# Kernel optimization log

Hardware: AMD Instinct MI355X
Metric: run time of the kernel (lower is better)

## Reference

```python
import jax, jax.numpy as jnp
import numpy as np

B, R, D = 16, 2048, 512
H2, NREL = 2 * D, 2048  # relation_mlp hidden = 2*d_model, output = n_relations
MIN_PROB = 0.1          # early-stop probability threshold from the torch code


def setup_inputs() -> dict:
    key = jax.random.key(0)
    ks = jax.random.split(key, 8)
    sc = lambda k, shp: jax.random.normal(k, shp, jnp.float32) * 0.02
    return {
        "rel_encoding": jax.random.normal(ks[0], (B, R, D), jnp.float32),
        "na_emb": jax.random.normal(ks[1], (D,), jnp.float32),
        "v_w": sc(ks[2], (D, D)), "v_b": jnp.zeros((D,), jnp.float32),
        "o_w": sc(ks[3], (D, D)), "o_b": jnp.zeros((D,), jnp.float32),
        "ln_g": jnp.ones((D,), jnp.float32), "ln_b": jnp.zeros((D,), jnp.float32),
        "w1": sc(ks[4], (H2, D)), "b1": jnp.zeros((H2,), jnp.float32),
        "w2": sc(ks[5], (NREL, H2)), "b2": jnp.zeros((NREL,), jnp.float32),
    }


def _ln(x, g, b, eps=1e-5):
    m = jnp.mean(x, axis=-1, keepdims=True)
    v = jnp.var(x, axis=-1, keepdims=True)
    return (x - m) * jax.lax.rsqrt(v + eps) * g + b


def reference(rel_encoding, na_emb, v_w, v_b, o_w, o_b, ln_g, ln_b, w1, b1, w2, b2):
    # Cross-attention with a single key/value token: softmax over a length-1 axis
    # is identically 1, so attn_out = out_proj(v_proj(kv)) for every query position.
    x = rel_encoding                                         # [B,R,D]
    attn = (x @ v_w.T + v_b) @ o_w.T + o_b                   # [B,R,D]

    def step_logits(state):                                  # state broadcasts to [B,R,D]
        h = _ln(attn + state, ln_g, ln_b)                    # residual + layernorm
        return jax.nn.relu(h @ w1.T + b1) @ w2.T + b2        # [B,R,NREL]

    # step 0: query is the na_embedding
    p0 = jax.nn.softmax(step_logits(na_emb), axis=-1)
    m0 = jnp.max(p0, axis=-1)
    i0 = jnp.argmax(p0, axis=-1)
    cont0 = (i0 != 0) & (m0 >= MIN_PROB)                     # else break before step 0 emits

    # step 1: last appended state is the relation encoding itself
    p1 = jax.nn.softmax(step_logits(x), axis=-1)
    m1 = jnp.max(p1, axis=-1)
    i1 = jnp.argmax(p1, axis=-1)
    cont1 = cont0 & (i1 != 0) & (m1 >= MIN_PROB)

    # rule_score = prod of accepted step probs; 0.0 if no step accepted
    scores = jnp.where(cont0, jnp.where(cont1, m0 * m1, m0), 0.0)  # [B,R]
    lengths = cont0.astype(jnp.int32) + cont1.astype(jnp.int32)    # ragged rule lengths
    return scores, i0, i1, lengths
```

## Files before the change

kernel.cpp:

```cpp
#include <hip/hip_runtime.h>
#include <math.h>

#define MTOT 32768
#define DD   512
#define HHD  1024
#define NRELN 2048
#define SCA  64.f
#define SCB  1024.f
#define INVS (1.f / 65536.f)
#define CAPR 4096
#define MARGIN 2.0e-3f

typedef _Float16 h8  __attribute__((ext_vector_type(8)));
typedef float    f4  __attribute__((ext_vector_type(4)));
typedef float    f16v __attribute__((ext_vector_type(16)));

__device__ __forceinline__ void fsplit(float x, _Float16& h, _Float16& l) {
  _Float16 t = (_Float16)x;
  h = t;
  l = (_Float16)(x - (float)t);
}

__device__ __forceinline__ void gld16(const _Float16* g, _Float16* l) {
  __builtin_amdgcn_global_load_lds(
      (const __attribute__((address_space(1))) void*)g,
      (__attribute__((address_space(3))) void*)l, 16, 0, 0);
}


__global__ void prep_wvo_split(const float* __restrict__ vw, const float* __restrict__ ow,
                               _Float16* __restrict__ wh, _Float16* __restrict__ wl) {
  int idx = blockIdx.x * 256 + threadIdx.x;
  int k = idx & 511;
  int n = idx >> 9;
  float s = 0.f;
  for (int j = 0; j < DD; ++j) s += ow[n * DD + j] * vw[j * DD + k];
  fsplit(s * SCB, wh[n * DD + k], wl[n * DD + k]);
}

__global__ void prep_cvec(const float* __restrict__ ow, const float* __restrict__ vb,
                          const float* __restrict__ ob, float* __restrict__ c) {
  int i = blockIdx.x * 256 + threadIdx.x;
  if (i < DD) {
    float s = ob[i];
    for (int k = 0; k < DD; ++k) s += ow[i * DD + k] * vb[k];
    c[i] = s;
  }
}

__global__ void prep_w1p_split(const float* __restrict__ w1, const float* __restrict__ g,
                               _Float16* __restrict__ wh, _Float16* __restrict__ wl) {
  int idx = blockIdx.x * 256 + threadIdx.x;
  int k = idx & 511;
  int n = idx >> 9;
  fsplit(w1[n * DD + k] * g[k] * SCB, wh[n * DD + k], wl[n * DD + k]);
}

__global__ void prep_b1p(const float* __restrict__ w1, const float* __restrict__ lnb,
                         const float* __restrict__ b1, float* __restrict__ b1p) {
  int n = blockIdx.x * 256 + threadIdx.x;
  if (n < HHD) {
    float s = b1[n];
    for (int k = 0; k < DD; ++k) s += w1[n * DD + k] * lnb[k];
    b1p[n] = s;
  }
}

__global__ void prep_w2_split(const float* __restrict__ w2,
                              _Float16* __restrict__ wh, _Float16* __restrict__ wl) {
  int idx = blockIdx.x * 256 + threadIdx.x;
  int k = idx & 1023;
  int n = idx >> 10;
  fsplit(w2[n * HHD + k] * SCB, wh[n * HHD + k], wl[n * HHD + k]);
}

__global__ void split_x(const float* __restrict__ src, _Float16* __restrict__ h,
                        _Float16* __restrict__ l) {
  int idx = (blockIdx.x * 256 + threadIdx.x) * 8;
  float4 a = *(const float4*)(src + idx);
  float4 b = *(const float4*)(src + idx + 4);
  float vv[8] = {a.x, a.y, a.z, a.w, b.x, b.y, b.z, b.w};
  _Float16 hh[8], ll[8];
#pragma unroll
  for (int i = 0; i < 8; ++i) fsplit(vv[i] * SCA, hh[i], ll[i]);
  *(h8*)(h + idx) = *(h8*)hh;
  *(h8*)(l + idx) = *(h8*)ll;
}

__global__ void zero_cnt(int* c) { c[blockIdx.x * 256 + threadIdx.x] = 0; }

template <int MODE, int KDIM, int NTOT>
__global__ __launch_bounds__(256) void gemm_split(
    const _Float16* __restrict__ Ah, const _Float16* __restrict__ Al,
    const _Float16* __restrict__ Bh, const _Float16* __restrict__ Bl,
    const float* __restrict__ bias,
    float* __restrict__ outF,
    _Float16* __restrict__ outHh, _Float16* __restrict__ outHl,
    float* __restrict__ pM, float* __restrict__ pI,
    const int* __restrict__ cntp, int pstr) {
  __shared__ __align__(16) _Float16 sA[2][128][32];
  __shared__ __align__(16) _Float16 sB[2][128][32];
  const int t = threadIdx.x;
  const int lane = t & 63;
  const int wv = t >> 6;
  const int wr = wv & 1, wc = wv >> 1;
  const int l31 = lane & 31, half = lane >> 5;
  const int n0 = blockIdx.y << 7;

  const _Float16* gsp = (wv == 0) ? Ah : (wv == 1) ? Al : (wv == 2) ? Bh : Bl;
  _Float16* lbase = (wv == 0) ? &sA[0][0][0] : (wv == 1) ? &sA[1][0][0]
                  : (wv == 2) ? &sB[0][0][0] : &sB[1][0][0];
  const int srow = lane >> 2;
  const int scp = lane & 3;
  const int swzE = ((srow >> 1) & 3) ^ ((srow >> 3) & 1);
  const int swzO = swzE ^ 2;
  const int swz = ((l31 >> 1) ^ (l31 >> 3)) & 3;

  int nmb;
  if constexpr (MODE == 2) {
    int a = *cntp;
    if (a > CAPR) a = CAPR;
    nmb = (a + 127) >> 7;
  } else {
    nmb = gridDim.x;
  }

  for (int mb = blockIdx.x; mb < nmb; mb += gridDim.x) {
    const int m0 = mb << 7;
    const int gb = (wv < 2) ? m0 : n0;
    const _Float16* gA0 = gsp + (size_t)(gb + srow) * KDIM + ((scp ^ swzE) << 3);
    const _Float16* gA1 = gsp + (size_t)(gb + srow) * KDIM + ((scp ^ swzO) << 3);

    f16v acc[2][2] = {};
    for (int k0 = 0; k0 < KDIM; k0 += 32) {
      __syncthreads();
#pragma unroll
      for (int it = 0; it < 8; ++it)
        gld16(((it & 1) ? gA1 : gA0) + (size_t)(it * 16) * KDIM + k0, lbase + it * 512);
      __syncthreads();
#pragma unroll
      for (int ks = 0; ks < 2; ++ks) {
        const int pos = (((ks << 1) + half) ^ swz) << 3;
        h8 af_h[2], af_l[2], bf_h[2], bf_l[2];
#pragma unroll
        for (int i = 0; i < 2; ++i) {
          const int mr = wr * 64 + i * 32 + l31;
          af_h[i] = *(const h8*)&sA[0][mr][pos];
          af_l[i] = *(const h8*)&sA[1][mr][pos];
        }
#pragma unroll
        for (int j = 0; j < 2; ++j) {
          const int nr = wc * 64 + j * 32 + l31;
          bf_h[j] = *(const h8*)&sB[0][nr][pos];
          bf_l[j] = *(const h8*)&sB[1][nr][pos];
        }
#pragma unroll
        for (int j = 0; j < 2; ++j)
#pragma unroll
          for (int i = 0; i < 2; ++i) {
            acc[i][j] = __builtin_amdgcn_mfma_f32_32x32x16_f16(af_h[i], bf_h[j], acc[i][j], 0, 0, 0);
            acc[i][j] = __builtin_amdgcn_mfma_f32_32x32x16_f16(af_h[i], bf_l[j], acc[i][j], 0, 0, 0);
            acc[i][j] = __builtin_amdgcn_mfma_f32_32x32x16_f16(af_l[i], bf_h[j], acc[i][j], 0, 0, 0);
          }
      }
    }

    float bb[2];
    int gc[2];
#pragma unroll
    for (int j = 0; j < 2; ++j) {
      gc[j] = n0 + wc * 64 + j * 32 + l31;
      bb[j] = bias[gc[j]];
    }
    if constexpr (MODE == 0) {
#pragma unroll
      for (int i = 0; i < 2; ++i)
#pragma unroll
        for (int r = 0; r < 16; ++r) {
          const int row = m0 + wr * 64 + i * 32 + (r & 3) + 8 * (r >> 2) + 4 * half;
#pragma unroll
          for (int j = 0; j < 2; ++j)
            outF[(size_t)row * NTOT + gc[j]] = acc[i][j][r] * INVS + bb[j];
        }
    } else if constexpr (MODE == 1) {
#pragma unroll
      for (int i = 0; i < 2; ++i)
#pragma unroll
        for (int r = 0; r < 16; ++r) {
          const int row = m0 + wr * 64 + i * 32 + (r & 3) + 8 * (r >> 2) + 4 * half;
#pragma unroll
          for (int j = 0; j < 2; ++j) {
            float v = fmaxf(acc[i][j][r] * INVS + bb[j], 0.f) * SCA;
            _Float16 hh, ll;
            fsplit(v, hh, ll);
            outHh[(size_t)row * NTOT + gc[j]] = hh;
            outHl[(size_t)row * NTOT + gc[j]] = ll;
          }
        }
    } else {
      const int slot = blockIdx.y * 2 + wc;
#pragma unroll
      for (int i = 0; i < 2; ++i)
#pragma unroll
        for (int r = 0; r < 16; ++r) {
          float v0 = acc[i][0][r] * INVS + bb[0];
          float v1 = acc[i][1][r] * INVS + bb[1];
          float M;
          int I;
          if (v0 >= v1) { M = v0; I = gc[0]; }
          else          { M = v1; I = gc[1]; }
#pragma unroll
          for (int sh = 1; sh <= 16; sh <<= 1) {
            float M2 = __shfl_xor(M, sh);
            int   I2 = __shfl_xor(I, sh);
            if (M2 > M || (M2 == M && I2 < I)) { M = M2; I = I2; }
          }
          if (l31 == 0) {
            const int grow = m0 + wr * 64 + i * 32 + (r & 3) + 8 * (r >> 2) + 4 * half;
            pM[(size_t)slot * pstr + grow] = M;
            pI[(size_t)slot * pstr + grow] = (float)I;
          }
        }
    }
  }
}


#define SBAR __builtin_amdgcn_s_barrier()
#define SCHB __builtin_amdgcn_sched_barrier(0)
#define LW0  asm volatile("s_waitcnt lgkmcnt(0)" ::: "memory")
#define VW(N) asm volatile("s_waitcnt vmcnt(" #N ")" ::: "memory")
#define VWNONE ((void)0)

#define GLB(k, ktn, nb_)                                                      \
  gld16(Bh + (size_t)(sBb + (k) * 16384 + (ktn) * 64),                        \
        lds + 32768 + dBb + (k) * 1024 + (nb_) * 16384)
#define GLA(k, ktn, nb_)                                                      \
  gld16(Ah + (size_t)(sAb + (k) * 32768 + (ktn) * 64),                        \
        lds + dAb + (k) * 2048 + (nb_) * 16384)

#define PHASE(p, cbuf, STAGE, VWS)                                            \
  {                                                                           \
    h8 a00 = *(const h8*)(lds + (cbuf) + aRow + (2 * (p)) * 1024 + kc0);      \
    h8 a01 = *(const h8*)(lds + (cbuf) + aRow + (2 * (p)) * 1024 + kc1);      \
    h8 a10 = *(const h8*)(lds + (cbuf) + aRow + (2 * (p) + 1) * 1024 + kc0);  \
    h8 a11 = *(const h8*)(lds + (cbuf) + aRow + (2 * (p) + 1) * 1024 + kc1);  \
    STAGE;                                                                    \
    SBAR;                                                                     \
    LW0;                                                                      \
    SCHB;                                                                     \
    __builtin_amdgcn_s_setprio(1);                                            \
    _Pragma("unroll") for (int j = 0; j < 4; ++j) {                           \
      acc[2 * (p)][j] = __builtin_amdgcn_mfma_f32_16x16x32_f16(               \
          a00, bf0[j], acc[2 * (p)][j], 0, 0, 0);                             \
      acc[2 * (p)][j] = __builtin_amdgcn_mfma_f32_16x16x32_f16(               \
          a01, bf1[j], acc[2 * (p)][j], 0, 0, 0);                             \
      acc[2 * (p) + 1][j] = __builtin_amdgcn_mfma_f32_16x16x32_f16(           \
          a10, bf0[j], acc[2 * (p) + 1][j], 0, 0, 0);                         \
      acc[2 * (p) + 1][j] = __builtin_amdgcn_mfma_f32_16x16x32_f16(           \
          a11, bf1[j], acc[2 * (p) + 1][j], 0, 0, 0);                         \
    }                                                                         \
    __builtin_amdgcn_s_setprio(0);                                            \
    VWS;                                                                      \
    SBAR;                                                                     \
  }

__global__ __launch_bounds__(512, 2) void gemm_approx(
    const _Float16* __restrict__ Ah, const _Float16* __restrict__ Bh,
    const float* __restrict__ bias,
    float* __restrict__ pM, float* __restrict__ pM2,
    float* __restrict__ pS, int* __restrict__ pI, int astr) {
  __shared__ __align__(16) _Float16 lds[65536];
  const int t = threadIdx.x;
  const int lane = t & 63;
  const int wv = t >> 6;
  const int wr = wv >> 2;
  const int wc = wv & 3;
  const int q = lane >> 4;
  const int l16 = lane & 15;
  const int s7 = l16 & 7;
  const int l8 = lane >> 3;
  const int lc = lane & 7;

  const int Yg = gridDim.y;
  const int id = blockIdx.x + (blockIdx.y << 3);
  const int g8 = (id >> 6) << 3;
  const int r = id & 63;
  int mb, nb;
  if (g8 + 8 <= Yg) { mb = g8 + (r & 7); nb = r >> 3; }
  else { int rem = Yg - g8; mb = g8 + (r % rem); nb = r / rem; }

  const int m0 = mb << 8;
  const int n0 = nb << 8;

  const int swz8 = (lc ^ l8) << 3;
  const int sBb = (n0 + wc * 64 + wr * 8 + l8) * HHD + swz8;
  const int dBb = (wc * 64 + wr * 8) * 64;
  const int sAb = (m0 + wr * 128 + wc * 8 + l8) * HHD + swz8;
  const int dAb = (wr * 128 + wc * 8) * 64;

  const int kc0 = ((q) ^ s7) << 3;
  const int kc1 = ((q + 4) ^ s7) << 3;
  const int aRow = (wr * 128 + l16) * 64;
  const int bRow = 32768 + (wc * 64 + l16) * 64;

  f4 acc[8][4] = {};

  GLB(0, 0, 0); GLB(1, 0, 0); GLB(2, 0, 0); GLB(3, 0, 0);
  GLA(0, 0, 0); GLA(1, 0, 0); GLA(2, 0, 0); GLA(3, 0, 0);
  VW(3);
  SBAR;

  for (int kt = 0; kt < 15; ++kt) {
    const int cb = (kt & 1) << 14;
    const int nbuf = (kt & 1) ^ 1;
    const int ktn = kt + 1;
    h8 bf0[4], bf1[4];
#pragma unroll
    for (int j = 0; j < 4; ++j) {
      bf0[j] = *(const h8*)(lds + cb + bRow + j * 1024 + kc0);
      bf1[j] = *(const h8*)(lds + cb + bRow + j * 1024 + kc1);
    }
    PHASE(0, cb, GLB(0, ktn, nbuf); GLB(1, ktn, nbuf), VW(4));
    PHASE(1, cb, GLB(2, ktn, nbuf); GLB(3, ktn, nbuf), VW(5));
    PHASE(2, cb, GLA(0, ktn, nbuf); GLA(1, ktn, nbuf), VW(6));
    PHASE(3, cb, GLA(2, ktn, nbuf); GLA(3, ktn, nbuf), VW(3));
  }
  {
    const int cb = 16384;
    h8 bf0[4], bf1[4];
#pragma unroll
    for (int j = 0; j < 4; ++j) {
      bf0[j] = *(const h8*)(lds + cb + bRow + j * 1024 + kc0);
      bf1[j] = *(const h8*)(lds + cb + bRow + j * 1024 + kc1);
    }
    PHASE(0, cb, VWNONE, VW(2));
    PHASE(1, cb, VWNONE, VW(1));
    PHASE(2, cb, VWNONE, VW(0));
    PHASE(3, cb, VWNONE, VWNONE);
  }

  const int slot = nb * 4 + wc;
  float bb[4];
  int gcx[4];
#pragma unroll
  for (int j = 0; j < 4; ++j) {
    gcx[j] = n0 + wc * 64 + j * 16 + l16;
    bb[j] = bias[gcx[j]];
  }
#pragma unroll
  for (int i = 0; i < 8; ++i)
#pragma unroll
    for (int rr = 0; rr < 4; ++rr) {
      float M = acc[i][0][rr] * INVS + bb[0], M2 = -INFINITY, S = 1.f;
      int I = gcx[0];
#pragma unroll
      for (int j = 1; j < 4; ++j) {
        float v = acc[i][j][rr] * INVS + bb[j];
        if (v > M || (v == M && gcx[j] < I)) {
          S = S * __expf(M - v) + 1.f; M2 = M; M = v; I = gcx[j];
        } else {
          S += __expf(v - M); M2 = fmaxf(M2, v);
        }
      }
#pragma unroll
      for (int sh = 1; sh <= 8; sh <<= 1) {
        float Mo = __shfl_xor(M, sh);
        float M2o = __shfl_xor(M2, sh);
        float So = __shfl_xor(S, sh);
        int   Io = __shfl_xor(I, sh);
        if (Mo > M || (Mo == M && Io < I)) {
          S = S * __expf(M - Mo) + So; M2 = fmaxf(M, M2o); M = Mo; I = Io;
        } else {
          S += So * __expf(Mo - M); M2 = fmaxf(M2, Mo);
        }
      }
      if (l16 == 0) {
        const int grow = m0 + wr * 128 + i * 16 + q * 4 + rr;
        pM[(size_t)slot * astr + grow] = M;
        pM2[(size_t)slot * astr + grow] = M2;
        pS[(size_t)slot * astr + grow] = S;
        pI[(size_t)slot * astr + grow] = I;
      }
    }
}

__global__ void flag_k(const float* __restrict__ pM, const float* __restrict__ pM2,
                       const float* __restrict__ pS, const int* __restrict__ pI,
                       int astr, int rows,
                       float* __restrict__ map, int* __restrict__ iap, int row0,
                       int* __restrict__ list, int* __restrict__ cnt) {
  int r = blockIdx.x * 256 + threadIdx.x;
  if (r >= rows) return;
  float M = pM[r], M2 = pM2[r], S = pS[r];
  int I = pI[r];
  for (int s = 1; s < 32; ++s) {
    size_t o = (size_t)s * astr + r;
    float m = pM[o], m2 = pM2[o], ss = pS[o];
    int ii = pI[o];
    if (m > M || (m == M && ii < I)) {
      M2 = fmaxf(M, m2); S = S * __expf(M - m) + ss; M = m; I = ii;
    } else {
      M2 = fmaxf(M2, m); S += ss * __expf(m - M);
    }
  }
  map[row0 + r] = 1.f / S;
  iap[row0 + r] = I;
  if (M - M2 < MARGIN) {
    int c = atomicAdd(cnt, 1);
    if (c < CAPR) list[c] = r;
  }
}

__global__ void gather_k(const _Float16* __restrict__ Hh, const _Float16* __restrict__ Hl,
                         const int* __restrict__ list, const int* __restrict__ cnt,
                         _Float16* __restrict__ Gh, _Float16* __restrict__ Gl) {
  int b = blockIdx.x;
  int active = *cnt;
  if (active > CAPR) active = CAPR;
  if (b >= active) return;
  int r = list[b];
  int t = threadIdx.x;
  *(h8*)(Gh + (size_t)b * HHD + t * 8) = *(const h8*)(Hh + (size_t)r * HHD + t * 8);
  *(h8*)(Gl + (size_t)b * HHD + t * 8) = *(const h8*)(Hl + (size_t)r * HHD + t * 8);
}

__global__ void rescue_merge(const float* __restrict__ pMr, const float* __restrict__ pIr,
                             const int* __restrict__ list, const int* __restrict__ cnt,
                             int* __restrict__ iap, int row0) {
  int c = blockIdx.x * 256 + threadIdx.x;
  int a = *cnt;
  if (a > CAPR) a = CAPR;
  if (c >= a) return;
  float M = pMr[c];
  int I = (int)pIr[c];
  for (int s = 1; s < 32; ++s) {
    size_t o = (size_t)s * CAPR + c;
    float m = pMr[o];
    int i2 = (int)pIr[o];
    if (m > M || (m == M && i2 < I)) { M = m; I = i2; }
  }
  iap[row0 + list[c]] = I;
}

__global__ __launch_bounds__(256) void ln_dual(
    const float* __restrict__ A, const float* __restrict__ X,
    const float* __restrict__ na,
    _Float16* __restrict__ y0h, _Float16* __restrict__ y0l,
    _Float16* __restrict__ y1h, _Float16* __restrict__ y1l) {
  int t = threadIdx.x;
  int lane = t & 63;
  int w = t >> 6;
  int r = blockIdx.x * 4 + w;
  const float* ap = A + (size_t)r * DD + lane * 8;
  const float* xp = X + (size_t)r * DD + lane * 8;
  const float* np = na + lane * 8;
  float v0[8], v1[8];
  float s0 = 0.f, q0 = 0.f, s1 = 0.f, q1 = 0.f;
#pragma unroll
  for (int i = 0; i < 8; ++i) {
    float a = ap[i];
    v0[i] = a + np[i];
    v1[i] = a + xp[i];
    s0 += v0[i]; q0 += v0[i] * v0[i];
    s1 += v1[i]; q1 += v1[i] * v1[i];
  }
#pragma unroll
  for (int m = 1; m <= 32; m <<= 1) {
    s0 += __shfl_xor(s0, m); q0 += __shfl_xor(q0, m);
    s1 += __shfl_xor(s1, m); q1 += __shfl_xor(q1, m);
  }
  float mu0 = s0 * (1.f / DD), mu1 = s1 * (1.f / DD);
  float rs0 = 1.f / sqrtf(q0 * (1.f / DD) - mu0 * mu0 + 1e-5f);
  float rs1 = 1.f / sqrtf(q1 * (1.f / DD) - mu1 * mu1 + 1e-5f);
  _Float16 h0[8], l0[8], h1[8], l1[8];
#pragma unroll
  for (int i = 0; i < 8; ++i) {
    fsplit((v0[i] - mu0) * rs0 * SCA, h0[i], l0[i]);
    fsplit((v1[i] - mu1) * rs1 * SCA, h1[i], l1[i]);
  }
  *(h8*)(y0h + (size_t)r * DD + lane * 8) = *(h8*)h0;
  *(h8*)(y0l + (size_t)r * DD + lane * 8) = *(h8*)l0;
  *(h8*)(y1h + (size_t)r * DD + lane * 8) = *(h8*)h1;
  *(h8*)(y1l + (size_t)r * DD + lane * 8) = *(h8*)l1;
}

__global__ void finalize_k(const float* __restrict__ map0, const int* __restrict__ iap0,
                           const float* __restrict__ map1, const int* __restrict__ iap1,
                           float* __restrict__ out) {
  int r = blockIdx.x * 256 + threadIdx.x;
  float m0v = map0[r], m1v = map1[r];
  int i0v = iap0[r], i1v = iap1[r];
  bool c0 = (i0v != 0) && (m0v >= 0.1f);
  bool c1 = c0 && (i1v != 0) && (m1v >= 0.1f);
  out[r] = c0 ? (c1 ? m0v * m1v : m0v) : 0.f;
  out[MTOT + r] = (float)i0v;
  out[2 * MTOT + r] = (float)i1v;
  out[3 * MTOT + r] = (float)((c0 ? 1 : 0) + (c1 ? 1 : 0));
}

extern "C" void kernel_launch(void* const* d_in, const int* in_sizes, int n_in,
                              void* d_out, int out_size, void* d_ws, size_t ws_size,
                              hipStream_t stream) {
  const float* X   = (const float*)d_in[0];
  const float* na  = (const float*)d_in[1];
  const float* vw  = (const float*)d_in[2];
  const float* vb  = (const float*)d_in[3];
  const float* ow  = (const float*)d_in[4];
  const float* ob  = (const float*)d_in[5];
  const float* lng = (const float*)d_in[6];
  const float* lnb = (const float*)d_in[7];
  const float* w1  = (const float*)d_in[8];
  const float* b1  = (const float*)d_in[9];
  const float* w2  = (const float*)d_in[10];
  const float* b2  = (const float*)d_in[11];
  float* out = (float*)d_out;

  char* p = (char*)d_ws;
  auto alloc = [&](size_t bytes) -> void* {
    void* r = (void*)p;
    p += (bytes + 255) & ~(size_t)255;
    return r;
  };
  _Float16* wvo_h = (_Float16*)alloc(512 * 512 * 2);
  _Float16* wvo_l = (_Float16*)alloc(512 * 512 * 2);
  float*    cvec  = (float*)alloc(512 * 4);
  _Float16* w1p_h = (_Float16*)alloc(1024 * 512 * 2);
  _Float16* w1p_l = (_Float16*)alloc(1024 * 512 * 2);
  float*    b1p   = (float*)alloc(1024 * 4);
  _Float16* w2_h  = (_Float16*)alloc(2048 * 1024 * 2);
  _Float16* w2_l  = (_Float16*)alloc(2048 * 1024 * 2);
  float* map0 = (float*)alloc((size_t)MTOT * 4);
  float* map1 = (float*)alloc((size_t)MTOT * 4);
  int* iap0 = (int*)alloc((size_t)MTOT * 4);
  int* iap1 = (int*)alloc((size_t)MTOT * 4);
  int* list = (int*)alloc(CAPR * 4);
  int* cnt  = (int*)alloc(512 * 4);
  float* pMr = (float*)alloc((size_t)32 * CAPR * 4);
  float* pIr = (float*)alloc((size_t)32 * CAPR * 4);
  _Float16* Gh = (_Float16*)alloc((size_t)CAPR * HHD * 2);
  _Float16* Gl = (_Float16*)alloc((size_t)CAPR * HHD * 2);

  size_t fixed = (size_t)(p - (char*)d_ws);
  size_t reserve = 2u << 20;
  size_t remain = ws_size > fixed + reserve ? ws_size - fixed - reserve : 0;
  int chunk = (int)(remain / 10752);
  chunk &= ~255;
  if (chunk < 256) chunk = 256;
  if (chunk > MTOT) chunk = MTOT;

  _Float16* xs_h = (_Float16*)alloc((size_t)chunk * 512 * 2);
  _Float16* xs_l = (_Float16*)alloc((size_t)chunk * 512 * 2);
  float*    Abuf = (float*)alloc((size_t)chunk * 512 * 4);
  _Float16* y0_h = (_Float16*)alloc((size_t)chunk * 512 * 2);
  _Float16* y0_l = (_Float16*)alloc((size_t)chunk * 512 * 2);
  _Float16* H_h  = (_Float16*)alloc((size_t)chunk * 1024 * 2);
  _Float16* H_l  = (_Float16*)alloc((size_t)chunk * 1024 * 2);
  float* pMa  = (float*)alloc((size_t)32 * chunk * 4);
  float* pM2a = (float*)alloc((size_t)32 * chunk * 4);
  float* pSa  = (float*)alloc((size_t)32 * chunk * 4);
  int*   pIa  = (int*)alloc((size_t)32 * chunk * 4);
  _Float16* y1_h = xs_h;
  _Float16* y1_l = xs_l;

  zero_cnt<<<2, 256, 0, stream>>>(cnt);
  prep_wvo_split<<<1024, 256, 0, stream>>>(vw, ow, wvo_h, wvo_l);
  prep_cvec<<<2, 256, 0, stream>>>(ow, vb, ob, cvec);
  prep_w1p_split<<<2048, 256, 0, stream>>>(w1, lng, w1p_h, w1p_l);
  prep_b1p<<<4, 256, 0, stream>>>(w1, lnb, b1, b1p);
  prep_w2_split<<<8192, 256, 0, stream>>>(w2, w2_h, w2_l);

  int citer = 0;
  for (int row0 = 0; row0 < MTOT; row0 += chunk, ++citer) {
    int rows = (MTOT - row0 < chunk) ? (MTOT - row0) : chunk;
    split_x<<<rows * 512 / 2048, 256, 0, stream>>>(X + (size_t)row0 * 512, xs_h, xs_l);
    gemm_split<0, 512, 512><<<dim3(rows / 128, 4), 256, 0, stream>>>(
        xs_h, xs_l, wvo_h, wvo_l, cvec, Abuf, nullptr, nullptr,
        nullptr, nullptr, nullptr, 0);
    ln_dual<<<rows / 4, 256, 0, stream>>>(Abuf, X + (size_t)row0 * 512, na,
                                          y0_h, y0_l, y1_h, y1_l);
    for (int s = 0; s < 2; ++s) {
      int* cp = cnt + citer * 2 + s;
      gemm_split<1, 512, 1024><<<dim3(rows / 128, 8), 256, 0, stream>>>(
          s == 0 ? y0_h : y1_h, s == 0 ? y0_l : y1_l, w1p_h, w1p_l, b1p,
          nullptr, H_h, H_l, nullptr, nullptr, nullptr, 0);
      gemm_approx<<<dim3(8, rows / 256), 512, 0, stream>>>(
          H_h, w2_h, b2, pMa, pM2a, pSa, pIa, chunk);
      flag_k<<<(rows + 255) / 256, 256, 0, stream>>>(
          pMa, pM2a, pSa, pIa, chunk, rows,
          s == 0 ? map0 : map1, s == 0 ? iap0 : iap1, row0, list, cp);
      gather_k<<<CAPR, 128, 0, stream>>>(H_h, H_l, list, cp, Gh, Gl);
      gemm_split<2, 1024, 2048><<<dim3(32, 16), 256, 0, stream>>>(
          Gh, Gl, w2_h, w2_l, b2, nullptr, nullptr, nullptr,
          pMr, pIr, cp, CAPR);
      rescue_merge<<<CAPR / 256, 256, 0, stream>>>(
          pMr, pIr, list, cp, s == 0 ? iap0 : iap1, row0);
    }
  }
  finalize_k<<<MTOT / 256, 256, 0, stream>>>(map0, iap0, map1, iap1, out);
}
```

Measured before the change: 1.555 ms.

## Replace double-buffered phased GEMM pipeline with single-buffer sync loop

```diff
diff --git a/kernel.cpp b/kernel.cpp
--- a/kernel.cpp
+++ b/kernel.cpp
@@ -226,51 +226,12 @@
 }
 
 
-#define SBAR __builtin_amdgcn_s_barrier()
-#define SCHB __builtin_amdgcn_sched_barrier(0)
-#define LW0  asm volatile("s_waitcnt lgkmcnt(0)" ::: "memory")
-#define VW(N) asm volatile("s_waitcnt vmcnt(" #N ")" ::: "memory")
-#define VWNONE ((void)0)
-
-#define GLB(k, ktn, nb_)                                                      \
-  gld16(Bh + (size_t)(sBb + (k) * 16384 + (ktn) * 64),                        \
-        lds + 32768 + dBb + (k) * 1024 + (nb_) * 16384)
-#define GLA(k, ktn, nb_)                                                      \
-  gld16(Ah + (size_t)(sAb + (k) * 32768 + (ktn) * 64),                        \
-        lds + dAb + (k) * 2048 + (nb_) * 16384)
-
-#define PHASE(p, cbuf, STAGE, VWS)                                            \
-  {                                                                           \
-    h8 a00 = *(const h8*)(lds + (cbuf) + aRow + (2 * (p)) * 1024 + kc0);      \
-    h8 a01 = *(const h8*)(lds + (cbuf) + aRow + (2 * (p)) * 1024 + kc1);      \
-    h8 a10 = *(const h8*)(lds + (cbuf) + aRow + (2 * (p) + 1) * 1024 + kc0);  \
-    h8 a11 = *(const h8*)(lds + (cbuf) + aRow + (2 * (p) + 1) * 1024 + kc1);  \
-    STAGE;                                                                    \
-    SBAR;                                                                     \
-    LW0;                                                                      \
-    SCHB;                                                                     \
-    __builtin_amdgcn_s_setprio(1);                                            \
-    _Pragma("unroll") for (int j = 0; j < 4; ++j) {                           \
-      acc[2 * (p)][j] = __builtin_amdgcn_mfma_f32_16x16x32_f16(               \
-          a00, bf0[j], acc[2 * (p)][j], 0, 0, 0);                             \
-      acc[2 * (p)][j] = __builtin_amdgcn_mfma_f32_16x16x32_f16(               \
-          a01, bf1[j], acc[2 * (p)][j], 0, 0, 0);                             \
-      acc[2 * (p) + 1][j] = __builtin_amdgcn_mfma_f32_16x16x32_f16(           \
-          a10, bf0[j], acc[2 * (p) + 1][j], 0, 0, 0);                         \
-      acc[2 * (p) + 1][j] = __builtin_amdgcn_mfma_f32_16x16x32_f16(           \
-          a11, bf1[j], acc[2 * (p) + 1][j], 0, 0, 0);                         \
-    }                                                                         \
-    __builtin_amdgcn_s_setprio(0);                                            \
-    VWS;                                                                      \
-    SBAR;                                                                     \
-  }
-
-__global__ __launch_bounds__(512, 2) void gemm_approx(
+__global__ __launch_bounds__(512, 4) void gemm_approx(
     const _Float16* __restrict__ Ah, const _Float16* __restrict__ Bh,
     const float* __restrict__ bias,
     float* __restrict__ pM, float* __restrict__ pM2,
     float* __restrict__ pS, int* __restrict__ pI, int astr) {
-  __shared__ __align__(16) _Float16 lds[65536];
+  __shared__ __align__(16) _Float16 lds[32768];
   const int t = threadIdx.x;
   const int lane = t & 63;
   const int wv = t >> 6;
@@ -302,42 +263,40 @@
   const int kc0 = ((q) ^ s7) << 3;
   const int kc1 = ((q + 4) ^ s7) << 3;
   const int aRow = (wr * 128 + l16) * 64;
-  const int bRow = 32768 + (wc * 64 + l16) * 64;
+  const int bRow = 16384 + (wc * 64 + l16) * 64;
 
   f4 acc[8][4] = {};
 
-  GLB(0, 0, 0); GLB(1, 0, 0); GLB(2, 0, 0); GLB(3, 0, 0);
-  GLA(0, 0, 0); GLA(1, 0, 0); GLA(2, 0, 0); GLA(3, 0, 0);
-  VW(3);
-  SBAR;
-
-  for (int kt = 0; kt < 15; ++kt) {
-    const int cb = (kt & 1) << 14;
-    const int nbuf = (kt & 1) ^ 1;
-    const int ktn = kt + 1;
+  for (int kt = 0; kt < 16; ++kt) {
+    __syncthreads();
+#pragma unroll
+    for (int k = 0; k < 4; ++k) {
+      gld16(Bh + (size_t)(sBb + k * 16384 + kt * 64), lds + 16384 + dBb + k * 1024);
+      gld16(Ah + (size_t)(sAb + k * 32768 + kt * 64), lds + dAb + k * 2048);
+    }
+    __syncthreads();
+    __builtin_amdgcn_s_setprio(1);
     h8 bf0[4], bf1[4];
 #pragma unroll
     for (int j = 0; j < 4; ++j) {
-      bf0[j] = *(const h8*)(lds + cb + bRow + j * 1024 + kc0);
-      bf1[j] = *(const h8*)(lds + cb + bRow + j * 1024 + kc1);
-    }
-    PHASE(0, cb, GLB(0, ktn, nbuf); GLB(1, ktn, nbuf), VW(4));
-    PHASE(1, cb, GLB(2, ktn, nbuf); GLB(3, ktn, nbuf), VW(5));
-    PHASE(2, cb, GLA(0, ktn, nbuf); GLA(1, ktn, nbuf), VW(6));
-    PHASE(3, cb, GLA(2, ktn, nbuf); GLA(3, ktn, nbuf), VW(3));
-  }
-  {
-    const int cb = 16384;
-    h8 bf0[4], bf1[4];
-#pragma unroll
-    for (int j = 0; j < 4; ++j) {
-      bf0[j] = *(const h8*)(lds + cb + bRow + j * 1024 + kc0);
-      bf1[j] = *(const h8*)(lds + cb + bRow + j * 1024 + kc1);
-    }
-    PHASE(0, cb, VWNONE, VW(2));
-    PHASE(1, cb, VWNONE, VW(1));
-    PHASE(2, cb, VWNONE, VW(0));
-    PHASE(3, cb, VWNONE, VWNONE);
+      bf0[j] = *(const h8*)(lds + bRow + j * 1024 + kc0);
+      bf1[j] = *(const h8*)(lds + bRow + j * 1024 + kc1);
+    }
+#pragma unroll
+    for (int p = 0; p < 4; ++p) {
+      h8 a00 = *(const h8*)(lds + aRow + (2 * p) * 1024 + kc0);
+      h8 a01 = *(const h8*)(lds + aRow + (2 * p) * 1024 + kc1);
+      h8 a10 = *(const h8*)(lds + aRow + (2 * p + 1) * 1024 + kc0);
+      h8 a11 = *(const h8*)(lds + aRow + (2 * p + 1) * 1024 + kc1);
+#pragma unroll
+      for (int j = 0; j < 4; ++j) {
+        acc[2 * p][j] = __builtin_amdgcn_mfma_f32_16x16x32_f16(a00, bf0[j], acc[2 * p][j], 0, 0, 0);
+        acc[2 * p][j] = __builtin_amdgcn_mfma_f32_16x16x32_f16(a01, bf1[j], acc[2 * p][j], 0, 0, 0);
+        acc[2 * p + 1][j] = __builtin_amdgcn_mfma_f32_16x16x32_f16(a10, bf0[j], acc[2 * p + 1][j], 0, 0, 0);
+        acc[2 * p + 1][j] = __builtin_amdgcn_mfma_f32_16x16x32_f16(a11, bf1[j], acc[2 * p + 1][j], 0, 0, 0);
+      }
+    }
+    __builtin_amdgcn_s_setprio(0);
   }
 
   const int slot = nb * 4 + wc;
```

New measurement: 3.912 ms. 2.52x slower.
